# Optimization experiments

Hardware: AMD Instinct MI355X
Metric: run time of the kernel (lower is better)

## Reference

```python
import jax, jax.numpy as jnp
import numpy as np

# raster settings (match init_kwargs)
H, W = 512, 512
TANFOVX, TANFOVY = 0.5, 0.5
DENSITY_SHIFT = -2.0
SCALE_MOD = 1.0
SH_DEG = 2
N, R, D = 262144, 8, 8

SH_C0 = 0.28209479177387814
SH_C1 = 0.4886025119029199
SH_C2 = (1.0925484305920792, -1.0925484305920792, 0.31539156525252005,
         -1.0925484305920792, 0.5462742152960396)


def _camera():
    # row-vector convention: p_view = p_world @ V[:3,:3] + V[3,:3]
    view = np.eye(4, dtype=np.float32)
    view[3, 2] = 3.0  # camera at (0,0,-3) looking down +z
    znear, zfar = 0.01, 100.0
    top, right = TANFOVY * znear, TANFOVX * znear
    P = np.zeros((4, 4), np.float32)
    P[0, 0] = znear / right
    P[1, 1] = znear / top
    P[2, 2] = zfar / (zfar - znear)
    P[2, 3] = 1.0
    P[3, 2] = -zfar * znear / (zfar - znear)
    proj = view @ P  # full world->clip, row-vector convention
    campos = np.array([0.0, 0.0, -3.0], np.float32)
    return jnp.asarray(view), jnp.asarray(proj), jnp.asarray(campos)


def setup_inputs() -> dict:
    key = jax.random.key(0)
    ks = jax.random.split(key, 6)
    positions = jax.random.uniform(ks[0], (N, 3), jnp.float32)          # local coords in [0,1]
    trivecs = jax.random.normal(ks[1], (N, R, 3, D), jnp.float32)
    densities = jax.random.normal(ks[2], (N, R), jnp.float32)
    shs = jax.random.normal(ks[3], (N, R, (SH_DEG + 1) ** 2, 3), jnp.float32) * 0.3
    view, proj, campos = _camera()
    aabb = jnp.array([-1.0, -1.0, -1.0, 2.0, 2.0, 2.0], jnp.float32)    # [origin, size]
    bg = jnp.zeros((3,), jnp.float32)
    rnd = jnp.full((H, W, 3), 0.5, jnp.float32)
    rnd = rnd.at[..., 2].set(jax.random.uniform(ks[4], (H, W), jnp.float32))
    return {"positions": positions, "trivecs": trivecs, "densities": densities,
            "shs": shs, "viewmatrix": view, "projmatrix": proj, "campos": campos,
            "aabb": aabb, "bg": bg, "random_image": rnd}


def _rasterize(positions, trivecs, densities, shs, viewmatrix, projmatrix, campos, aabb, bg):
    world = aabb[:3] + positions * aabb[3:]                              # [N,3]
    ones = jnp.ones((world.shape[0], 1), world.dtype)
    ph = jnp.concatenate([world, ones], 1) @ projmatrix                  # [N,4]
    ndc = ph[:, :3] / (ph[:, 3:4] + 1e-7)
    pview = world @ viewmatrix[:3, :3] + viewmatrix[3, :3]
    depth = pview[:, 2]                                                  # [N]
    ix = jnp.round(((ndc[:, 0] + 1.0) * W - 1.0) * 0.5).astype(jnp.int32)
    iy = jnp.round(((ndc[:, 1] + 1.0) * H - 1.0) * 0.5).astype(jnp.int32)
    valid = (depth > 0.2) & (ix >= 0) & (ix < W) & (iy >= 0) & (iy < H)
    pid = jnp.where(valid, iy * W + ix, H * W)                           # dump bucket H*W

    # trivec density at the cell center: product of the three axis vectors
    mid = trivecs[:, :, :, D // 2]                                       # [N,R,3]
    tri = jax.nn.relu(jnp.prod(mid, axis=-1))                            # [N,R]
    sigma_r = jnp.exp(densities + DENSITY_SHIFT) * tri * SCALE_MOD       # [N,R]
    sigma = sigma_r.sum(-1)
    alpha = jnp.clip(1.0 - jnp.exp(-sigma), 0.0, 0.999)                  # [N]

    # per-rank SH color, density-weighted over ranks
    dirs = world - campos
    dirs = dirs / (jnp.linalg.norm(dirs, axis=-1, keepdims=True) + 1e-8)
    x, y, z = dirs[:, 0:1], dirs[:, 1:2], dirs[:, 2:3]
    basis = jnp.concatenate([
        jnp.full_like(x, SH_C0),
        -SH_C1 * y, SH_C1 * z, -SH_C1 * x,
        SH_C2[0] * x * y, SH_C2[1] * y * z,
        SH_C2[2] * (2.0 * z * z - x * x - y * y),
        SH_C2[3] * x * z, SH_C2[4] * (x * x - y * y)], axis=1)           # [N,9]
    color_r = jnp.maximum(jnp.einsum('nk,nrkc->nrc', basis, shs) + 0.5, 0.0)
    wr = sigma_r / (sigma + 1e-8)[:, None]
    color = jnp.einsum('nr,nrc->nc', wr, color_r)                        # [N,3]

    # depth-sorted per-pixel alpha compositing via segmented exclusive cumsum
    order = jnp.lexsort((depth, pid))
    pid_s, a_s = pid[order], alpha[order]
    c_s, d_s = color[order], depth[order]
    logs = jnp.log1p(-a_s)
    excl = jnp.cumsum(logs) - logs                                       # exclusive cumsum
    first = jnp.searchsorted(pid_s, pid_s, side='left')                  # segment start idx
    T = jnp.exp(excl - excl[first])                                      # transmittance
    wgt = a_s * T
    npx = H * W
    img_c = jax.ops.segment_sum(wgt[:, None] * c_s, pid_s, num_segments=npx + 1)[:npx]
    img_a = jax.ops.segment_sum(wgt, pid_s, num_segments=npx + 1)[:npx]
    img_d = jax.ops.segment_sum(wgt * d_s, pid_s, num_segments=npx + 1)[:npx]
    img_c = img_c + (1.0 - img_a)[:, None] * bg
    pct_d = img_d / (img_a + 1e-8)
    return (img_c.reshape(H, W, 3).transpose(2, 0, 1),
            img_d.reshape(H, W), img_a.reshape(H, W), pct_d.reshape(H, W))


def reference(positions, trivecs, densities, shs, viewmatrix, projmatrix, campos, aabb, bg, random_image):
    # random_image is only used for stochastic jitter in the CUDA kernel; deterministic here
    return _rasterize(positions, trivecs, densities, shs, viewmatrix, projmatrix, campos, aabb, bg)
```

## Files before the change

### kernel.cpp

```cpp
#include <hip/hip_runtime.h>
#include <math.h>
#include <float.h>

#define Hh 512
#define Ww 512
#define HWW (Hh*Ww)
#define NP 262144
#define KMAX 16


__device__ __forceinline__ unsigned long long umin64(unsigned long long a,
                                                     unsigned long long b){
    return a < b ? a : b;
}

__global__ __launch_bounds__(256) void point_kernel(
    const float* __restrict__ positions,
    const float* __restrict__ trivecs,
    const float* __restrict__ densities,
    const float* __restrict__ shs,
    const float* __restrict__ viewm,
    const float* __restrict__ projm,
    const float* __restrict__ campos,
    const float* __restrict__ aabb,
    float* __restrict__ recs,
    int* __restrict__ heads)
{
#pragma clang fp contract(off)
    int gid = blockIdx.x * blockDim.x + threadIdx.x;
    int n    = gid >> 1;
    int half = gid & 1;

    float px = positions[n*3+0], py = positions[n*3+1], pz = positions[n*3+2];

    float4 dv = *(const float4*)(densities + (size_t)n*8 + half*4);

    const float* tv = trivecs + (size_t)n*192 + half*96;
    float tvm[12];
    #pragma unroll
    for (int r = 0; r < 4; r++){
        tvm[r*3+0] = tv[r*24 + 4];
        tvm[r*3+1] = tv[r*24 + 12];
        tvm[r*3+2] = tv[r*24 + 20];
    }

    const float4* sp = (const float4*)(shs + (size_t)n*216) + half*27;
    float4 sh[27];
    #pragma unroll
    for (int j = 0; j < 27; j++) sh[j] = sp[j];

    float wx = aabb[0] + px*aabb[3];
    float wy = aabb[1] + py*aabb[4];
    float wz = aabb[2] + pz*aabb[5];

    float phx = ((wx*projm[0] + wy*projm[4]) + wz*projm[8])  + projm[12];
    float phy = ((wx*projm[1] + wy*projm[5]) + wz*projm[9])  + projm[13];
    float phw = ((wx*projm[3] + wy*projm[7]) + wz*projm[11]) + projm[15];
    float denom = phw + 1e-7f;
    float ndcx = phx / denom;
    float ndcy = phy / denom;
    float depth = ((wx*viewm[2] + wy*viewm[6]) + wz*viewm[10]) + viewm[14];

    float fx = ((ndcx + 1.0f)*(float)Ww - 1.0f)*0.5f;
    float fy = ((ndcy + 1.0f)*(float)Hh - 1.0f)*0.5f;
    int ix = (int)rintf(fx);
    int iy = (int)rintf(fy);
    bool valid = (depth > 0.2f) && (ix >= 0) && (ix < Ww) && (iy >= 0) && (iy < Hh);
    int pid = valid ? (iy*Ww + ix) : -1;

    float den[4] = {dv.x, dv.y, dv.z, dv.w};
    float sr[4]; float sig_half = 0.0f;
    #pragma unroll
    for (int r = 0; r < 4; r++){
        float tri = tvm[r*3+0]*tvm[r*3+1]*tvm[r*3+2];
        tri = tri > 0.0f ? tri : 0.0f;
        float s = expf(den[r] - 2.0f) * tri;
        sr[r] = s; sig_half += s;
    }
    float sigma = sig_half + __shfl_xor(sig_half, 1, 64);
    float alpha = 1.0f - expf(-sigma);
    alpha = fminf(alpha, 0.999f);
    alpha = fmaxf(alpha, 0.0f);

    float dxr = wx - campos[0], dyr = wy - campos[1], dzr = wz - campos[2];
    float nrm = sqrtf((dxr*dxr + dyr*dyr) + dzr*dzr) + 1e-8f;
    float x = dxr/nrm, y = dyr/nrm, z = dzr/nrm;
    float basis[9];
    basis[0] = 0.28209479177387814f;
    basis[1] = -0.4886025119029199f * y;
    basis[2] =  0.4886025119029199f * z;
    basis[3] = -0.4886025119029199f * x;
    basis[4] =  1.0925484305920792f * (x*y);
    basis[5] = -1.0925484305920792f * (y*z);
    basis[6] =  0.31539156525252005f * (2.0f*z*z - x*x - y*y);
    basis[7] = -1.0925484305920792f * (x*z);
    basis[8] =  0.5462742152960396f * (x*x - y*y);

    float dot[4][3];
    #pragma unroll
    for (int r = 0; r < 4; r++){ dot[r][0]=0.f; dot[r][1]=0.f; dot[r][2]=0.f; }
    #pragma unroll
    for (int j = 0; j < 27; j++){
        float e[4] = {sh[j].x, sh[j].y, sh[j].z, sh[j].w};
        #pragma unroll
        for (int q = 0; q < 4; q++){
            int f = 4*j + q;
            int r = f / 27;
            int k = (f % 27) / 3;
            int c = f % 3;
            dot[r][c] = fmaf(basis[k], e[q], dot[r][c]);
        }
    }
    float invs = 1.0f/(sigma + 1e-8f);
    float cr = 0.f, cg = 0.f, cb = 0.f;
    #pragma unroll
    for (int r = 0; r < 4; r++){
        float wr = sr[r]*invs;
        cr = fmaf(wr, fmaxf(dot[r][0] + 0.5f, 0.0f), cr);
        cg = fmaf(wr, fmaxf(dot[r][1] + 0.5f, 0.0f), cg);
        cb = fmaf(wr, fmaxf(dot[r][2] + 0.5f, 0.0f), cb);
    }
    cr += __shfl_xor(cr, 1, 64);
    cg += __shfl_xor(cg, 1, 64);
    cb += __shfl_xor(cb, 1, 64);

    if (half == 0 && pid >= 0){
        int next = atomicExch(&heads[pid], n);
        float4* rp = (float4*)(recs + (size_t)n*8);
        rp[0] = make_float4(depth, __int_as_float(next), alpha, cr);
        *(float2*)(recs + (size_t)n*8 + 4) = make_float2(cg, cb);
    }
}

__global__ __launch_bounds__(256) void composite_kernel(
    const int* __restrict__ heads,
    const float* __restrict__ recs,
    const float* __restrict__ bg,
    float* __restrict__ out)
{
    int p = blockIdx.x * blockDim.x + threadIdx.x;
    if (p >= HWW) return;

    const unsigned long long NONE = ~0ull;
    unsigned long long keys[KMAX];
    int cur = heads[p];

    #pragma unroll
    for (int i = 0; i < KMAX; i++){
        unsigned long long k = NONE;
        if (cur >= 0){
            float2 dn = *(const float2*)(recs + (size_t)cur*8);
            k = ((unsigned long long)__float_as_uint(dn.x) << 32) |
                (unsigned int)cur;
            cur = __float_as_int(dn.y);
        }
        keys[i] = k;
    }
    bool overflow = (cur >= 0);

    float T = 1.0f, accA = 0.f, accD = 0.f, aR = 0.f, aG = 0.f, aB = 0.f;

    if (!overflow){
        for (int it = 0; it < KMAX; ++it){
            unsigned long long m0 = umin64(keys[0],  keys[1]);
            unsigned long long m1 = umin64(keys[2],  keys[3]);
            unsigned long long m2 = umin64(keys[4],  keys[5]);
            unsigned long long m3 = umin64(keys[6],  keys[7]);
            unsigned long long m4 = umin64(keys[8],  keys[9]);
            unsigned long long m5 = umin64(keys[10], keys[11]);
            unsigned long long m6 = umin64(keys[12], keys[13]);
            unsigned long long m7 = umin64(keys[14], keys[15]);
            m0 = umin64(m0, m1); m2 = umin64(m2, m3);
            m4 = umin64(m4, m5); m6 = umin64(m6, m7);
            m0 = umin64(m0, m2); m4 = umin64(m4, m6);
            unsigned long long m = umin64(m0, m4);

            if (!__any(m != NONE)) break;

            if (m != NONE){
                int nidx = (int)(m & 0xffffffffu);
                float4 ra = *(const float4*)(recs + (size_t)nidx*8);
                float2 rb = *(const float2*)(recs + (size_t)nidx*8 + 4);
                float a = ra.z, w = a*T;
                aR += w*ra.w; aG += w*rb.x; aB += w*rb.y;
                accA += w; accD += w*ra.x;
                T *= (1.0f - a);
                #pragma unroll
                for (int j = 0; j < KMAX; j++)
                    keys[j] = (keys[j] == m) ? NONE : keys[j];
            }
        }
    } else {
        unsigned long long last = 0; bool haveLast = false;
        for (;;){
            unsigned long long best = NONE;
            for (int c2 = heads[p]; c2 >= 0; ){
                float2 dn = *(const float2*)(recs + (size_t)c2*8);
                unsigned long long k =
                    ((unsigned long long)__float_as_uint(dn.x) << 32) |
                    (unsigned int)c2;
                if ((!haveLast || k > last) && k < best) best = k;
                c2 = __float_as_int(dn.y);
            }
            if (best == NONE) break;
            int nidx = (int)(best & 0xffffffffu);
            float4 ra = *(const float4*)(recs + (size_t)nidx*8);
            float2 rb = *(const float2*)(recs + (size_t)nidx*8 + 4);
            float a = ra.z, w = a*T;
            aR += w*ra.w; aG += w*rb.x; aB += w*rb.y;
            accA += w; accD += w*ra.x;
            T *= (1.0f - a);
            last = best; haveLast = true;
        }
    }

    float om = 1.0f - accA;
    out[p]         = aR + om*bg[0];
    out[HWW + p]   = aG + om*bg[1];
    out[2*HWW + p] = aB + om*bg[2];
    out[3*HWW + p] = accD;
    out[4*HWW + p] = accA;
    out[5*HWW + p] = accD/(accA + 1e-8f);
}

extern "C" void kernel_launch(void* const* d_in, const int* in_sizes, int n_in,
                              void* d_out, int out_size, void* d_ws, size_t ws_size,
                              hipStream_t stream)
{
    const float* positions = (const float*)d_in[0];
    const float* trivecs   = (const float*)d_in[1];
    const float* densities = (const float*)d_in[2];
    const float* shs       = (const float*)d_in[3];
    const float* viewm     = (const float*)d_in[4];
    const float* projm     = (const float*)d_in[5];
    const float* campos    = (const float*)d_in[6];
    const float* aabb      = (const float*)d_in[7];
    const float* bg        = (const float*)d_in[8];
    float* out = (float*)d_out;

    char* ws = (char*)d_ws;
    size_t o = 0;
    int*   heads = (int*)(ws + o);   o += (size_t)HWW*4;
    float* recs  = (float*)(ws + o); o += (size_t)NP*32;

    hipMemsetAsync(heads, 0xFF, (size_t)HWW*4, stream);
    point_kernel<<<(NP*2)/256, 256, 0, stream>>>(positions, trivecs, densities, shs,
                                                 viewm, projm, campos, aabb,
                                                 recs, heads);
    composite_kernel<<<HWW/256, 256, 0, stream>>>(heads, recs, bg, out);
}
```

Before: 503.2 us.

## Map eight threads per point and stage SH coefficients through shared memory

Each point is now handled by eight threads, one per rank, instead of two. Each block cooperatively loads its 32 points' SH coefficients into LDS with fully coalesced float4 loads. Per-rank density and color sums are reduced with three xor shuffles. This is meant to remove the strided, register-heavy per-thread loads of 27 float4s and raise occupancy, at the cost of a block barrier, 27 KB of LDS per block and more shuffles.

```diff
diff --git a/kernel.cpp b/kernel.cpp
--- a/kernel.cpp
+++ b/kernel.cpp
@@ -7,6 +7,7 @@
 #define HWW (Hh*Ww)
 #define NP 262144
 #define KMAX 16
+#define PPB 32
 
 
 __device__ __forceinline__ unsigned long long umin64(unsigned long long a,
@@ -27,27 +28,40 @@
     int* __restrict__ heads)
 {
 #pragma clang fp contract(off)
-    int gid = blockIdx.x * blockDim.x + threadIdx.x;
-    int n    = gid >> 1;
-    int half = gid & 1;
+    __shared__ float4 sh4[PPB*54];
+
+    const int tid = threadIdx.x;
+    const int n0  = blockIdx.x * PPB;
+    const int p   = tid >> 3;
+    const int r   = tid & 7;
+    const int n   = n0 + p;
+
+    const float4* gsh = (const float4*)(shs + (size_t)n0*216);
+    float4 sb0 = gsh[tid];
+    float4 sb1 = gsh[tid +  256];
+    float4 sb2 = gsh[tid +  512];
+    float4 sb3 = gsh[tid +  768];
+    float4 sb4 = gsh[tid + 1024];
+    float4 sb5 = gsh[tid + 1280];
+    float4 sb6;
+    const int  i6   = tid + 1536;
+    const bool has6 = (i6 < 1728);
+    if (has6) sb6 = gsh[i6];
+
+    float den = densities[(size_t)n0*8 + tid];
+
+    const float* tv = trivecs + (size_t)n*192 + r*24;
+    float m0 = tv[4], m1 = tv[12], m2 = tv[20];
 
     float px = positions[n*3+0], py = positions[n*3+1], pz = positions[n*3+2];
 
-    float4 dv = *(const float4*)(densities + (size_t)n*8 + half*4);
-
-    const float* tv = trivecs + (size_t)n*192 + half*96;
-    float tvm[12];
-    #pragma unroll
-    for (int r = 0; r < 4; r++){
-        tvm[r*3+0] = tv[r*24 + 4];
-        tvm[r*3+1] = tv[r*24 + 12];
-        tvm[r*3+2] = tv[r*24 + 20];
-    }
-
-    const float4* sp = (const float4*)(shs + (size_t)n*216) + half*27;
-    float4 sh[27];
-    #pragma unroll
-    for (int j = 0; j < 27; j++) sh[j] = sp[j];
+    sh4[tid]        = sb0;
+    sh4[tid +  256] = sb1;
+    sh4[tid +  512] = sb2;
+    sh4[tid +  768] = sb3;
+    sh4[tid + 1024] = sb4;
+    sh4[tid + 1280] = sb5;
+    if (has6) sh4[i6] = sb6;
 
     float wx = aabb[0] + px*aabb[3];
     float wy = aabb[1] + py*aabb[4];
@@ -68,17 +82,14 @@
     bool valid = (depth > 0.2f) && (ix >= 0) && (ix < Ww) && (iy >= 0) && (iy < Hh);
     int pid = valid ? (iy*Ww + ix) : -1;
 
-    float den[4] = {dv.x, dv.y, dv.z, dv.w};
-    float sr[4]; float sig_half = 0.0f;
-    #pragma unroll
-    for (int r = 0; r < 4; r++){
-        float tri = tvm[r*3+0]*tvm[r*3+1]*tvm[r*3+2];
-        tri = tri > 0.0f ? tri : 0.0f;
-        float s = expf(den[r] - 2.0f) * tri;
-        sr[r] = s; sig_half += s;
-    }
-    float sigma = sig_half + __shfl_xor(sig_half, 1, 64);
-    float alpha = 1.0f - expf(-sigma);
+    float tri = m0*m1*m2;
+    tri = tri > 0.0f ? tri : 0.0f;
+    float s = expf(den - 2.0f) * tri;
+    float sig = s;
+    sig += __shfl_xor(sig, 1, 64);
+    sig += __shfl_xor(sig, 2, 64);
+    sig += __shfl_xor(sig, 4, 64);
+    float alpha = 1.0f - expf(-sig);
     alpha = fminf(alpha, 0.999f);
     alpha = fmaxf(alpha, 0.0f);
 
@@ -96,35 +107,27 @@
     basis[7] = -1.0925484305920792f * (x*z);
     basis[8] =  0.5462742152960396f * (x*x - y*y);
 
-    float dot[4][3];
+    __syncthreads();
+
+    const float* shr = (const float*)sh4 + p*216 + r*27;
+    float d0 = 0.f, d1 = 0.f, d2 = 0.f;
     #pragma unroll
-    for (int r = 0; r < 4; r++){ dot[r][0]=0.f; dot[r][1]=0.f; dot[r][2]=0.f; }
-    #pragma unroll
-    for (int j = 0; j < 27; j++){
-        float e[4] = {sh[j].x, sh[j].y, sh[j].z, sh[j].w};
-        #pragma unroll
-        for (int q = 0; q < 4; q++){
-            int f = 4*j + q;
-            int r = f / 27;
-            int k = (f % 27) / 3;
-            int c = f % 3;
-            dot[r][c] = fmaf(basis[k], e[q], dot[r][c]);
-        }
-    }
-    float invs = 1.0f/(sigma + 1e-8f);
-    float cr = 0.f, cg = 0.f, cb = 0.f;
-    #pragma unroll
-    for (int r = 0; r < 4; r++){
-        float wr = sr[r]*invs;
-        cr = fmaf(wr, fmaxf(dot[r][0] + 0.5f, 0.0f), cr);
-        cg = fmaf(wr, fmaxf(dot[r][1] + 0.5f, 0.0f), cg);
-        cb = fmaf(wr, fmaxf(dot[r][2] + 0.5f, 0.0f), cb);
-    }
-    cr += __shfl_xor(cr, 1, 64);
-    cg += __shfl_xor(cg, 1, 64);
-    cb += __shfl_xor(cb, 1, 64);
-
-    if (half == 0 && pid >= 0){
+    for (int k = 0; k < 9; k++){
+        float b = basis[k];
+        d0 = fmaf(b, shr[3*k+0], d0);
+        d1 = fmaf(b, shr[3*k+1], d1);
+        d2 = fmaf(b, shr[3*k+2], d2);
+    }
+    float invs = 1.0f/(sig + 1e-8f);
+    float wr = s*invs;
+    float cr = wr*fmaxf(d0 + 0.5f, 0.0f);
+    float cg = wr*fmaxf(d1 + 0.5f, 0.0f);
+    float cb = wr*fmaxf(d2 + 0.5f, 0.0f);
+    cr += __shfl_xor(cr, 1, 64); cr += __shfl_xor(cr, 2, 64); cr += __shfl_xor(cr, 4, 64);
+    cg += __shfl_xor(cg, 1, 64); cg += __shfl_xor(cg, 2, 64); cg += __shfl_xor(cg, 4, 64);
+    cb += __shfl_xor(cb, 1, 64); cb += __shfl_xor(cb, 2, 64); cb += __shfl_xor(cb, 4, 64);
+
+    if (r == 0 && pid >= 0){
         int next = atomicExch(&heads[pid], n);
         float4* rp = (float4*)(recs + (size_t)n*8);
         rp[0] = make_float4(depth, __int_as_float(next), alpha, cr);
@@ -244,8 +247,8 @@
     float* recs  = (float*)(ws + o); o += (size_t)NP*32;
 
     hipMemsetAsync(heads, 0xFF, (size_t)HWW*4, stream);
-    point_kernel<<<(NP*2)/256, 256, 0, stream>>>(positions, trivecs, densities, shs,
-                                                 viewm, projm, campos, aabb,
-                                                 recs, heads);
+    point_kernel<<<NP/PPB, 256, 0, stream>>>(positions, trivecs, densities, shs,
+                                             viewm, projm, campos, aabb,
+                                             recs, heads);
     composite_kernel<<<HWW/256, 256, 0, stream>>>(heads, recs, bg, out);
 }
```

Result: faster. 460.7 us (-8.4%).
